# Kernel optimization log

Hardware: AMD Instinct MI355X
Metric: run time of the kernel (lower is better)

## Reference

```python
import jax, jax.numpy as jnp
import numpy as np

N, E, D = 50000, 400000, 64
L, NA, NS = 5, 4, 3            # layers, num aggregators, num scalers
ATOM_C, ATOM_V = 9, 64         # OGB-style atom feature columns / vocab
BOND_C, BOND_V = 3, 8
EPS = 1e-5
AVG_LOG = float(np.log(9.0))   # avg_d['log'] = ln(avg_degree + 1), avg_degree = 8


def setup_inputs() -> dict:
    key = jax.random.key(0)
    ks = jax.random.split(key, 8)
    x = jax.random.randint(ks[0], (N, ATOM_C), 0, ATOM_V)
    edge_index = jax.random.randint(ks[1], (2, E), 0, N)
    edge_attr = jax.random.randint(ks[2], (E, BOND_C), 0, BOND_V)
    init = lambda k, shape, fan: (jax.random.normal(k, shape, jnp.float32) / np.sqrt(fan))
    atom_emb = init(ks[3], (ATOM_C, ATOM_V, D), D)
    bond_emb = init(ks[4], (BOND_C, BOND_V, D), D)
    pre_W = init(ks[5], (L, 3 * D, D), 3 * D)                 # pretrans: Linear(3D -> D)
    pre_b = jnp.zeros((L, D), jnp.float32)
    post_W = init(ks[6], (L, (NA * NS + 1) * D, D), (NA * NS + 1) * D)  # posttrans: Linear(13D -> D)
    post_b = jnp.zeros((L, D), jnp.float32)
    return dict(x=x, edge_index=edge_index, edge_attr=edge_attr,
                atom_emb=atom_emb, bond_emb=bond_emb,
                pre_W=pre_W, pre_b=pre_b, post_W=post_W, post_b=post_b)


def reference(x, edge_index, edge_attr, atom_emb, bond_emb, pre_W, pre_b, post_W, post_b):
    src, dst = edge_index[0], edge_index[1]  # PyG: x_j = x[edge_index[0]], x_i = x[edge_index[1]]
    # Encoders: sum of per-column categorical embeddings (OGB Atom/BondEncoder)
    h0 = atom_emb[jnp.arange(ATOM_C)[None, :], x].sum(axis=1)        # [N, D]
    e = bond_emb[jnp.arange(BOND_C)[None, :], edge_attr].sum(axis=1)  # [E, D]
    # message input cat([x_i, x_j, edge_attr]) -- identical for every layer since
    # PNAGNN.forward never feeds layer output back in as x (faithful to source)
    z2 = jnp.concatenate([h0[dst], h0[src], e], axis=-1)              # [E, 3D]
    deg = jax.ops.segment_sum(jnp.ones((E,), jnp.float32), dst, num_segments=N)
    degc = jnp.maximum(deg, 1.0)[:, None]
    log_deg = jnp.log(jnp.maximum(deg, 1.0) + 1.0)[:, None]           # guard deg=0 for attenuation
    amp = log_deg / AVG_LOG
    att = AVG_LOG / log_deg
    has = (deg > 0)[:, None]
    h_in = h0
    for l in range(L):
        m = z2 @ pre_W[l] + pre_b[l]                                  # pretrans (1 layer, no act)
        s_sum = jax.ops.segment_sum(m, dst, num_segments=N)
        mean = s_sum / degc
        mx = jnp.where(has, jax.ops.segment_max(m, dst, num_segments=N), 0.0)
        mn = jnp.where(has, jax.ops.segment_min(m, dst, num_segments=N), 0.0)
        mean_sq = jax.ops.segment_sum(m * m, dst, num_segments=N) / degc
        var = jax.nn.relu(mean_sq - mean * mean)
        std = jnp.sqrt(var + EPS)
        agg = jnp.concatenate([mean, mx, mn, std], axis=-1)           # [N, 4D]
        scaled = jnp.concatenate([agg, agg * amp, agg * att], axis=-1)  # [N, 12D]
        hcat = jnp.concatenate([scaled, h0], axis=-1)                 # [N, 13D]
        out = hcat @ post_W[l] + post_b[l]                            # posttrans (1 layer, no act)
        h = out + h_in                                                # PNAGNN residual
        h_in = h
    return h
```

## Files before the change

kernel.cpp:

```cpp
#include <hip/hip_runtime.h>
#include <hip/hip_bf16.h>

#define NN 50000
#define NE 400000
#define AVG_LOG_F 2.1972245773362196f
#define EPSV 1e-5f

typedef __hip_bfloat16 bf16;
typedef __attribute__((ext_vector_type(8))) short short8v;
typedef __attribute__((ext_vector_type(4))) float f32x4;
typedef __attribute__((ext_vector_type(2))) _Float16 h2v;

__device__ __forceinline__ float b2f(bf16 v){ return __bfloat162float(v); }
__device__ __forceinline__ bf16  f2b(float v){ return __float2bfloat16(v); }
__device__ __forceinline__ short f2s(float v){
  bf16 b = __float2bfloat16(v);
  short s; __builtin_memcpy(&s, &b, 2); return s;
}
__device__ __forceinline__ short f2h(float v){
  _Float16 h = (_Float16)v;
  short s; __builtin_memcpy(&s, &h, 2); return s;
}

__global__ void k_h0(const int* __restrict__ x, const float* __restrict__ aemb,
                     bf16* __restrict__ h0b){
  int idx = blockIdx.x * 256 + threadIdx.x;
  if (idx >= NN * 64) return;
  int n = idx >> 6, d = idx & 63;
  float acc = 0.f;
  #pragma unroll
  for (int c = 0; c < 9; ++c){
    int a = x[n * 9 + c];
    acc += aemb[(c * 64 + a) * 64 + d];
  }
  h0b[idx] = f2b(acc);
}

__global__ void k_deg_code(const int* __restrict__ ei, const int* __restrict__ ea,
                           int* __restrict__ deg, int* __restrict__ code){
  int e = blockIdx.x * 256 + threadIdx.x;
  if (e >= NE) return;
  int dst = ei[NE + e];
  atomicAdd(&deg[dst], 1);
  code[e] = ea[e * 3] + 8 * ea[e * 3 + 1] + 64 * ea[e * 3 + 2];
}

__global__ void k_scan1(const int* __restrict__ deg, int* __restrict__ rowptr,
                        int* __restrict__ part){
  __shared__ int s[256];
  int t = threadIdx.x, i = blockIdx.x * 256 + t;
  int v = (i < NN) ? deg[i] : 0;
  s[t] = v; __syncthreads();
  for (int off = 1; off < 256; off <<= 1){
    int xv = (t >= off) ? s[t - off] : 0;
    __syncthreads();
    s[t] += xv;
    __syncthreads();
  }
  if (i < NN) rowptr[i] = s[t] - v;
  if (t == 255) part[blockIdx.x] = s[255];
}

__global__ void k_scan2(int* __restrict__ part, int nblk){
  __shared__ int s[256];
  int t = threadIdx.x;
  int v = (t < nblk) ? part[t] : 0;
  s[t] = v; __syncthreads();
  for (int off = 1; off < 256; off <<= 1){
    int xv = (t >= off) ? s[t - off] : 0;
    __syncthreads();
    s[t] += xv;
    __syncthreads();
  }
  if (t < nblk) part[t] = s[t] - v;
}

__global__ void k_scan3(int* __restrict__ rowptr, const int* __restrict__ part,
                        const int* __restrict__ deg, float* __restrict__ amp,
                        float* __restrict__ att){
  int i = blockIdx.x * 256 + threadIdx.x;
  if (i < NN){
    rowptr[i] += part[blockIdx.x];
    int d = deg[i];
    float ld = logf((float)max(d, 1) + 1.0f);
    amp[i] = ld / AVG_LOG_F;
    att[i] = AVG_LOG_F / ld;
  }
  if (i == 0) rowptr[NN] = NE;
}

__global__ void k_scatter(const int* __restrict__ ei, const int* __restrict__ code,
                          const int* __restrict__ rowptr, int* __restrict__ cursor,
                          int2* __restrict__ sedge){
  int e = blockIdx.x * 256 + threadIdx.x;
  if (e >= NE) return;
  int dst = ei[NE + e];
  int pos = rowptr[dst] + atomicAdd(&cursor[dst], 1);
  int2 v; v.x = ei[e] * 1280; v.y = code[e] * 640;
  sedge[pos] = v;
}

__global__ void k_ctab(const float* __restrict__ bemb, const float* __restrict__ preW,
                       _Float16* __restrict__ CTp){
  __shared__ float et[64];
  int cb = blockIdx.x, l = blockIdx.y, t = threadIdx.x;
  int a0 = cb & 7, a1 = (cb >> 3) & 7, a2 = (cb >> 6) & 7;
  et[t] = bemb[(0 * 8 + a0) * 64 + t] + bemb[(1 * 8 + a1) * 64 + t] + bemb[(2 * 8 + a2) * 64 + t];
  __syncthreads();
  float acc = 0.f;
  const float* W = preW + (l * 192 + 128) * 64;
  for (int k = 0; k < 64; ++k) acc += et[k] * W[k * 64 + t];
  char* base = (char*)CTp + (size_t)cb * 640;
  if (l < 4) *(short*)(base + t * 8 + l * 2) = f2h(acc);
  else       *(short*)(base + 512 + t * 2)   = f2h(acc);
}

__global__ void k_whsum(const float* __restrict__ postW, const float* __restrict__ postb,
                        float* __restrict__ whs, float* __restrict__ bs){
  int idx = blockIdx.x * 256 + threadIdx.x;
  if (idx < 4096){
    int k = idx >> 6, d = idx & 63;
    float a = 0.f;
    for (int l = 0; l < 5; ++l) a += postW[(size_t)(l * 832 + 768 + k) * 64 + d];
    whs[idx] = a;
  }
  if (idx < 64){
    float a = 0.f;
    for (int l = 0; l < 5; ++l) a += postb[l * 64 + idx];
    bs[idx] = a;
  }
}

__global__ void k_wtk(const float* __restrict__ postW, bf16* __restrict__ WtKf){
  int idx = blockIdx.x * 256 + threadIdx.x;
  if (idx >= 40 * 12 * 64 * 8) return;
  int s   = idx / 6144;
  int rem = idx % 6144;
  int gw  = rem / 512;
  int lane = (rem % 512) / 8;
  int j   = idx & 7;
  int g = gw >> 2, w4 = gw & 3;
  int kp = s * 32 + (lane >> 4) * 8 + j;
  int l = kp >> 8, kl = kp & 255;
  int c = w4 * 16 + (lane & 15);
  WtKf[idx] = f2b(postW[((size_t)l * 832 + g * 256 + kl) * 64 + c]);
}

__global__ void k_wtpre896(const float* __restrict__ preW, const float* __restrict__ preb,
                           const float* __restrict__ whs, const float* __restrict__ bs,
                           bf16* __restrict__ Wtp, float* __restrict__ bias896){
  int idx = blockIdx.x * 256 + threadIdx.x;
  if (idx < 896 * 64){
    int gc = idx >> 6, k = idx & 63;
    float v;
    if (gc < 320){
      int l = gc >> 6, c = gc & 63;
      v = preW[(size_t)(l * 192 + k) * 64 + c];
    } else if (gc < 832){
      int q = gc - 320, d = q >> 3, l = q & 7;
      v = (l < 5) ? preW[(size_t)(l * 192 + 64 + k) * 64 + d] : 0.f;
    } else {
      int c = gc - 832;
      v = whs[k * 64 + c] + ((k == c) ? 1.f : 0.f);
    }
    Wtp[idx] = f2b(v);
  }
  if (idx < 896){
    float b;
    if (idx < 320)      b = preb[(idx >> 6) * 64 + (idx & 63)];
    else if (idx < 832) b = 0.f;
    else                b = bs[idx - 832];
    bias896[idx] = b;
  }
}

__global__ __launch_bounds__(256) void k_ab_mfma(const bf16* __restrict__ h0b,
                                                 const bf16* __restrict__ Wtp,
                                                 const float* __restrict__ bias896,
                                                 char* __restrict__ ABU,
                                                 float* __restrict__ out){
  __shared__ bf16 As[128][72];
  __shared__ bf16 Bs[128][72];
  const int t = threadIdx.x;
  const int n0 = blockIdx.x * 128;
  const int gc0 = blockIdx.y * 128;
  const int lane = t & 63, wid = t >> 6;
  const int rw = wid * 32;
  const short* H  = (const short*)h0b;
  const short* Wp = (const short*)Wtp;

  #pragma unroll
  for (int i = 0; i < 4; ++i){
    int idx = t + i * 256;
    int r = idx >> 3, ko = (idx & 7) * 8;
    int n = n0 + r;
    short8v v = short8v{0,0,0,0,0,0,0,0};
    if (n < NN) v = *(const short8v*)(H + (size_t)n * 64 + ko);
    *(short8v*)&As[r][ko] = v;
  }
  #pragma unroll
  for (int i = 0; i < 4; ++i){
    int idx = t + i * 256;
    int cc = idx >> 3, ko = (idx & 7) * 8;
    *(short8v*)&Bs[cc][ko] = *(const short8v*)(Wp + (size_t)(gc0 + cc) * 64 + ko);
  }
  __syncthreads();

  f32x4 acc[2][8] = {};
  #pragma unroll
  for (int kk = 0; kk < 2; ++kk){
    short8v af0 = *(const short8v*)&As[rw + (lane & 15)][kk * 32 + (lane >> 4) * 8];
    short8v af1 = *(const short8v*)&As[rw + 16 + (lane & 15)][kk * 32 + (lane >> 4) * 8];
    #pragma unroll
    for (int j = 0; j < 8; ++j){
      short8v bfj = *(const short8v*)&Bs[j * 16 + (lane & 15)][kk * 32 + (lane >> 4) * 8];
      acc[0][j] = __builtin_amdgcn_mfma_f32_16x16x32_bf16(af0, bfj, acc[0][j], 0, 0, 0);
      acc[1][j] = __builtin_amdgcn_mfma_f32_16x16x32_bf16(af1, bfj, acc[1][j], 0, 0, 0);
    }
  }

  #pragma unroll
  for (int i = 0; i < 2; ++i){
    #pragma unroll
    for (int r = 0; r < 4; ++r){
      int n = n0 + rw + i * 16 + (lane >> 4) * 4 + r;
      if (n >= NN) continue;
      char* nb = ABU + (size_t)n * 1280;
      #pragma unroll
      for (int j = 0; j < 8; ++j){
        int gc = gc0 + j * 16 + (lane & 15);
        float v = acc[i][j][r] + bias896[gc];
        if (gc < 320){
          *(short*)(nb + gc * 2) = f2h(v);
        } else if (gc < 832){
          int q = gc - 320, dd = q >> 3, l = q & 7;
          if (l < 4)       *(short*)(nb + 640 + dd * 8 + l * 2) = f2h(v);
          else if (l == 4) *(short*)(nb + 1152 + dd * 2)        = f2h(v);
        } else {
          out[(size_t)n * 64 + (gc - 832)] = v;
        }
      }
    }
  }
}

__global__ __launch_bounds__(256) void k_gather(const char* __restrict__ ABU,
                                                const char* __restrict__ CTp,
                                                const int* __restrict__ rowptr,
                                                const int2* __restrict__ sedge,
                                                bf16* __restrict__ AGG){
  const int t = threadIdx.x, lane = t & 63, wid = t >> 6;
  const int n = blockIdx.x * 4 + wid;
  const char* AB8 = ABU + 640;
  const char* AB2 = ABU + 1152;
  const char* CT8 = CTp;
  const char* CT2 = CTp + 512;
  short* AGs = (short*)AGG;

  int r0 = rowptr[n], r1 = rowptr[n + 1];
  float s[5]  = {0.f, 0.f, 0.f, 0.f, 0.f};
  float sq[5] = {0.f, 0.f, 0.f, 0.f, 0.f};
  const _Float16 FLO = (_Float16)(-65504.f);
  const _Float16 FHI = (_Float16)( 65504.f);
  h2v mx01 = h2v{FLO, FLO}, mx23 = h2v{FLO, FLO};
  h2v mn01 = h2v{FHI, FHI}, mn23 = h2v{FHI, FHI};
  float mx4 = -65504.f, mn4 = 65504.f;

  union U8 { uint2 u; h2v h[2]; };
  const int l8 = lane * 8, l2 = lane * 2;

  for (int j = r0; j < r1; j += 4){
    int rem = r1 - j;
    int2 e0 = sedge[j];
    int2 e1 = (rem > 1) ? sedge[j + 1] : e0;
    int2 e2 = (rem > 2) ? sedge[j + 2] : e0;
    int2 e3 = (rem > 3) ? sedge[j + 3] : e0;
    U8 a0, a1, a2, a3, c0, c1, c2, c3;
    unsigned short b0, b1, b2, b3, d0, d1, d2, d3;
    a0.u = *(const uint2*)(AB8 + e0.x + l8);  b0 = *(const unsigned short*)(AB2 + e0.x + l2);
    c0.u = *(const uint2*)(CT8 + e0.y + l8);  d0 = *(const unsigned short*)(CT2 + e0.y + l2);
    a1.u = *(const uint2*)(AB8 + e1.x + l8);  b1 = *(const unsigned short*)(AB2 + e1.x + l2);
    c1.u = *(const uint2*)(CT8 + e1.y + l8);  d1 = *(const unsigned short*)(CT2 + e1.y + l2);
    a2.u = *(const uint2*)(AB8 + e2.x + l8);  b2 = *(const unsigned short*)(AB2 + e2.x + l2);
    c2.u = *(const uint2*)(CT8 + e2.y + l8);  d2 = *(const unsigned short*)(CT2 + e2.y + l2);
    a3.u = *(const uint2*)(AB8 + e3.x + l8);  b3 = *(const unsigned short*)(AB2 + e3.x + l2);
    c3.u = *(const uint2*)(CT8 + e3.y + l8);  d3 = *(const unsigned short*)(CT2 + e3.y + l2);

    #define EDGE_ACC(A, C, BL, DL) {                                \
      h2v t01 = A.h[0] + C.h[0];                                    \
      h2v t23 = A.h[1] + C.h[1];                                    \
      _Float16 hb, hd;                                              \
      __builtin_memcpy(&hb, &BL, 2);                                \
      __builtin_memcpy(&hd, &DL, 2);                                \
      float f4 = (float)(hb + hd);                                  \
      mx01 = __builtin_elementwise_max(mx01, t01);                  \
      mx23 = __builtin_elementwise_max(mx23, t23);                  \
      mn01 = __builtin_elementwise_min(mn01, t01);                  \
      mn23 = __builtin_elementwise_min(mn23, t23);                  \
      mx4 = fmaxf(mx4, f4); mn4 = fminf(mn4, f4);                   \
      float f0 = (float)t01[0], f1 = (float)t01[1];                 \
      float f2 = (float)t23[0], f3 = (float)t23[1];                 \
      s[0] += f0; sq[0] = fmaf(f0, f0, sq[0]);                      \
      s[1] += f1; sq[1] = fmaf(f1, f1, sq[1]);                      \
      s[2] += f2; sq[2] = fmaf(f2, f2, sq[2]);                      \
      s[3] += f3; sq[3] = fmaf(f3, f3, sq[3]);                      \
      s[4] += f4; sq[4] = fmaf(f4, f4, sq[4]);                      \
    }
    EDGE_ACC(a0, c0, b0, d0);
    if (rem > 1) EDGE_ACC(a1, c1, b1, d1);
    if (rem > 2) EDGE_ACC(a2, c2, b2, d2);
    if (rem > 3) EDGE_ACC(a3, c3, b3, d3);
    #undef EDGE_ACC
  }

  float mx[5] = {(float)mx01[0], (float)mx01[1], (float)mx23[0], (float)mx23[1], mx4};
  float mn[5] = {(float)mn01[0], (float)mn01[1], (float)mn23[0], (float)mn23[1], mn4};

  int d = r1 - r0;
  float degc = (float)((d > 0) ? d : 1);
  size_t base = (size_t)n * 1280;
  const char* nb = ABU + (size_t)n * 1280;
  #pragma unroll
  for (int l = 0; l < 5; ++l){
    _Float16 Kh; __builtin_memcpy(&Kh, nb + l * 128 + lane * 2, 2);
    float K = (float)Kh;
    float mean = ((float)d * K + s[l]) / degc;
    float MX = (d > 0) ? (K + mx[l]) : 0.f;
    float MN = (d > 0) ? (K + mn[l]) : 0.f;
    float mu = s[l] / degc;
    float var = fmaxf(sq[l] / degc - mu * mu, 0.f);
    float sd = sqrtf(var + EPSV);
    AGs[base + l * 256 + lane]       = f2s(mean);
    AGs[base + l * 256 + 64 + lane]  = f2s(MX);
    AGs[base + l * 256 + 128 + lane] = f2s(MN);
    AGs[base + l * 256 + 192 + lane] = f2s(sd);
  }
}

__global__ __launch_bounds__(256) void k_post5(const bf16* __restrict__ AGG,
                                               const bf16* __restrict__ WtKf,
                                               const float* __restrict__ amp,
                                               const float* __restrict__ att,
                                               float* __restrict__ out){
  const int t = threadIdx.x, lane = t & 63, w4 = t >> 6;
  const int rg0 = blockIdx.x * 2;
  const char* pa0 = (const char*)AGG +
      ((size_t)(rg0 * 16) + (lane & 15)) * 2560 + (lane >> 4) * 16;
  const char* pa1 = pa0 + 16 * 2560;
  const char* pb  = (const char*)WtKf + w4 * 1024 + lane * 16;

  f32x4 acc[2][3] = {};
  short8v A0a, A1a, B0a, B1a, B2a, A0b, A1b, B0b, B1b, B2b;
  A0a = *(const short8v*)pa0;
  A1a = *(const short8v*)pa1;
  B0a = *(const short8v*)pb;
  B1a = *(const short8v*)(pb + 4096);
  B2a = *(const short8v*)(pb + 8192);

  #define MFMA6(A0, A1, B0, B1, B2)                                          \
    acc[0][0] = __builtin_amdgcn_mfma_f32_16x16x32_bf16(A0, B0, acc[0][0], 0, 0, 0); \
    acc[0][1] = __builtin_amdgcn_mfma_f32_16x16x32_bf16(A0, B1, acc[0][1], 0, 0, 0); \
    acc[0][2] = __builtin_amdgcn_mfma_f32_16x16x32_bf16(A0, B2, acc[0][2], 0, 0, 0); \
    acc[1][0] = __builtin_amdgcn_mfma_f32_16x16x32_bf16(A1, B0, acc[1][0], 0, 0, 0); \
    acc[1][1] = __builtin_amdgcn_mfma_f32_16x16x32_bf16(A1, B1, acc[1][1], 0, 0, 0); \
    acc[1][2] = __builtin_amdgcn_mfma_f32_16x16x32_bf16(A1, B2, acc[1][2], 0, 0, 0);

  for (int k = 0; k < 19; ++k){
    A0b = *(const short8v*)(pa0 + 64);
    A1b = *(const short8v*)(pa1 + 64);
    B0b = *(const short8v*)(pb + 12288);
    B1b = *(const short8v*)(pb + 12288 + 4096);
    B2b = *(const short8v*)(pb + 12288 + 8192);
    MFMA6(A0a, A1a, B0a, B1a, B2a);
    pa0 += 128; pa1 += 128; pb += 24576;
    A0a = *(const short8v*)pa0;
    A1a = *(const short8v*)pa1;
    B0a = *(const short8v*)pb;
    B1a = *(const short8v*)(pb + 4096);
    B2a = *(const short8v*)(pb + 8192);
    MFMA6(A0b, A1b, B0b, B1b, B2b);
  }
  A0b = *(const short8v*)(pa0 + 64);
  A1b = *(const short8v*)(pa1 + 64);
  B0b = *(const short8v*)(pb + 12288);
  B1b = *(const short8v*)(pb + 12288 + 4096);
  B2b = *(const short8v*)(pb + 12288 + 8192);
  MFMA6(A0a, A1a, B0a, B1a, B2a);
  MFMA6(A0b, A1b, B0b, B1b, B2b);
  #undef MFMA6

  #pragma unroll
  for (int i = 0; i < 2; ++i){
    #pragma unroll
    for (int r = 0; r < 4; ++r){
      int n = (rg0 + i) * 16 + (lane >> 4) * 4 + r;
      if (n >= NN) continue;
      float am = amp[n], at = att[n];
      int c = w4 * 16 + (lane & 15);
      out[(size_t)n * 64 + c] += acc[i][0][r] + am * acc[i][1][r] + at * acc[i][2][r];
    }
  }
}

extern "C" void kernel_launch(void* const* d_in, const int* in_sizes, int n_in,
                              void* d_out, int out_size, void* d_ws, size_t ws_size,
                              hipStream_t stream){
  const int*   x     = (const int*)d_in[0];
  const int*   ei    = (const int*)d_in[1];
  const int*   ea    = (const int*)d_in[2];
  const float* aemb  = (const float*)d_in[3];
  const float* bemb  = (const float*)d_in[4];
  const float* preW  = (const float*)d_in[5];
  const float* preb  = (const float*)d_in[6];
  const float* postW = (const float*)d_in[7];
  const float* postb = (const float*)d_in[8];
  float* out = (float*)d_out;

  char* p = (char*)d_ws;
  auto alloc = [&](size_t bytes) -> char* {
    char* r = p;
    p += (bytes + 255) & ~(size_t)255;
    return r;
  };
  bf16*      h0b     = (bf16*)     alloc((size_t)NN * 64 * 2);
  char*      ABU     = (char*)     alloc((size_t)NN * 1280);
  bf16*      AGG     = (bf16*)     alloc((size_t)(NN + 16) * 1280 * 2);
  int*       deg     = (int*)      alloc((size_t)NN * 4);
  int*       rowptr  = (int*)      alloc((size_t)(NN + 1) * 4);
  int*       cursor  = (int*)      alloc((size_t)NN * 4);
  float*     amp     = (float*)    alloc((size_t)NN * 4);
  float*     att     = (float*)    alloc((size_t)NN * 4);
  int*       code    = (int*)      alloc((size_t)NE * 4);
  int2*      sedge   = (int2*)     alloc((size_t)NE * 8);
  _Float16*  CTp     = (_Float16*) alloc((size_t)512 * 640);
  float*     whs     = (float*)    alloc((size_t)64 * 64 * 4);
  float*     bs      = (float*)    alloc((size_t)64 * 4);
  int*       part    = (int*)      alloc((size_t)256 * 4);
  bf16*      WtKf    = (bf16*)     alloc((size_t)40 * 12 * 64 * 8 * 2);
  bf16*      Wtp     = (bf16*)     alloc((size_t)896 * 64 * 2);
  float*     bias896 = (float*)    alloc((size_t)896 * 4);
  if ((size_t)(p - (char*)d_ws) > ws_size) return;

  hipMemsetAsync(deg, 0, (size_t)NN * 4, stream);
  hipMemsetAsync(cursor, 0, (size_t)NN * 4, stream);

  k_h0<<<dim3((NN * 64 + 255) / 256), 256, 0, stream>>>(x, aemb, h0b);
  k_deg_code<<<dim3((NE + 255) / 256), 256, 0, stream>>>(ei, ea, deg, code);
  int nblk = (NN + 255) / 256;
  k_scan1<<<dim3(nblk), 256, 0, stream>>>(deg, rowptr, part);
  k_scan2<<<dim3(1), 256, 0, stream>>>(part, nblk);
  k_scan3<<<dim3(nblk), 256, 0, stream>>>(rowptr, part, deg, amp, att);
  k_scatter<<<dim3((NE + 255) / 256), 256, 0, stream>>>(ei, code, rowptr, cursor, sedge);
  k_ctab<<<dim3(512, 5), 64, 0, stream>>>(bemb, preW, CTp);
  k_whsum<<<dim3(16), 256, 0, stream>>>(postW, postb, whs, bs);
  k_wtk<<<dim3((40 * 12 * 64 * 8 + 255) / 256), 256, 0, stream>>>(postW, WtKf);
  k_wtpre896<<<dim3((896 * 64 + 255) / 256), 256, 0, stream>>>(preW, preb, whs, bs,
                                                               Wtp, bias896);
  k_ab_mfma<<<dim3((NN + 127) / 128, 7), 256, 0, stream>>>(h0b, Wtp, bias896, ABU, out);
  k_gather<<<dim3(NN / 4), 256, 0, stream>>>(ABU, (const char*)CTp, rowptr, sedge, AGG);
  k_post5<<<dim3((3125 + 1) / 2), 256, 0, stream>>>(AGG, WtKf, amp, att, out);
}
```

Baseline: 312.9 us.

## Store aggregates in MFMA fragment order and widen post GEMM tile to 64 rows

The gather kernel now handles 16 nodes per 1024-thread block, stages each node's aggregate row in shared memory, and writes it out pre-swizzled into the MFMA A-fragment layout, so the post GEMM reads fully contiguous 1 KB chunks instead of strided rows. The post GEMM covers four 16-row groups per block instead of two, so each loaded weight fragment is reused across more rows, with double-buffered register loads. The aim is to cut uncoalesced A loads and redundant weight traffic. In exchange it adds a shared-memory staging step with a block barrier, larger blocks in the gather, more accumulator registers, and a padded workspace buffer.

```diff
diff --git a/kernel.cpp b/kernel.cpp
--- a/kernel.cpp
+++ b/kernel.cpp
@@ -244,18 +244,18 @@
   }
 }
 
-__global__ __launch_bounds__(256) void k_gather(const char* __restrict__ ABU,
-                                                const char* __restrict__ CTp,
-                                                const int* __restrict__ rowptr,
-                                                const int2* __restrict__ sedge,
-                                                bf16* __restrict__ AGG){
+__global__ __launch_bounds__(1024, 8) void k_gather(const char* __restrict__ ABU,
+                                                    const char* __restrict__ CTp,
+                                                    const int* __restrict__ rowptr,
+                                                    const int2* __restrict__ sedge,
+                                                    bf16* __restrict__ AGGf){
+  __shared__ __align__(16) short ag[16][1288];
   const int t = threadIdx.x, lane = t & 63, wid = t >> 6;
-  const int n = blockIdx.x * 4 + wid;
+  const int n = blockIdx.x * 16 + wid;
   const char* AB8 = ABU + 640;
   const char* AB2 = ABU + 1152;
   const char* CT8 = CTp;
   const char* CT2 = CTp + 512;
-  short* AGs = (short*)AGG;
 
   int r0 = rowptr[n], r1 = rowptr[n + 1];
   float s[5]  = {0.f, 0.f, 0.f, 0.f, 0.f};
@@ -318,7 +318,6 @@
 
   int d = r1 - r0;
   float degc = (float)((d > 0) ? d : 1);
-  size_t base = (size_t)n * 1280;
   const char* nb = ABU + (size_t)n * 1280;
   #pragma unroll
   for (int l = 0; l < 5; ++l){
@@ -330,74 +329,79 @@
     float mu = s[l] / degc;
     float var = fmaxf(sq[l] / degc - mu * mu, 0.f);
     float sd = sqrtf(var + EPSV);
-    AGs[base + l * 256 + lane]       = f2s(mean);
-    AGs[base + l * 256 + 64 + lane]  = f2s(MX);
-    AGs[base + l * 256 + 128 + lane] = f2s(MN);
-    AGs[base + l * 256 + 192 + lane] = f2s(sd);
-  }
-}
-
-__global__ __launch_bounds__(256) void k_post5(const bf16* __restrict__ AGG,
-                                               const bf16* __restrict__ WtKf,
-                                               const float* __restrict__ amp,
-                                               const float* __restrict__ att,
-                                               float* __restrict__ out){
+    ag[wid][l * 256 + lane]       = f2s(mean);
+    ag[wid][l * 256 + 64 + lane]  = f2s(MX);
+    ag[wid][l * 256 + 128 + lane] = f2s(MN);
+    ag[wid][l * 256 + 192 + lane] = f2s(sd);
+  }
+  __syncthreads();
+
+  char* dst = (char*)AGGf + (size_t)blockIdx.x * 40960;
+  for (int c = t; c < 2560; c += 1024){
+    int ln = c & 63;
+    int row = ln & 15;
+    int k = (c >> 6) * 32 + (ln >> 4) * 8;
+    short8v v = *(const short8v*)&ag[row][k];
+    *(short8v*)(dst + (size_t)c * 16) = v;
+  }
+}
+
+__global__ __launch_bounds__(256, 2) void k_post5(const bf16* __restrict__ AGGf,
+                                                  const bf16* __restrict__ WtKf,
+                                                  const float* __restrict__ amp,
+                                                  const float* __restrict__ att,
+                                                  float* __restrict__ out){
   const int t = threadIdx.x, lane = t & 63, w4 = t >> 6;
-  const int rg0 = blockIdx.x * 2;
-  const char* pa0 = (const char*)AGG +
-      ((size_t)(rg0 * 16) + (lane & 15)) * 2560 + (lane >> 4) * 16;
-  const char* pa1 = pa0 + 16 * 2560;
-  const char* pb  = (const char*)WtKf + w4 * 1024 + lane * 16;
-
-  f32x4 acc[2][3] = {};
-  short8v A0a, A1a, B0a, B1a, B2a, A0b, A1b, B0b, B1b, B2b;
-  A0a = *(const short8v*)pa0;
-  A1a = *(const short8v*)pa1;
-  B0a = *(const short8v*)pb;
-  B1a = *(const short8v*)(pb + 4096);
-  B2a = *(const short8v*)(pb + 8192);
-
-  #define MFMA6(A0, A1, B0, B1, B2)                                          \
-    acc[0][0] = __builtin_amdgcn_mfma_f32_16x16x32_bf16(A0, B0, acc[0][0], 0, 0, 0); \
-    acc[0][1] = __builtin_amdgcn_mfma_f32_16x16x32_bf16(A0, B1, acc[0][1], 0, 0, 0); \
-    acc[0][2] = __builtin_amdgcn_mfma_f32_16x16x32_bf16(A0, B2, acc[0][2], 0, 0, 0); \
-    acc[1][0] = __builtin_amdgcn_mfma_f32_16x16x32_bf16(A1, B0, acc[1][0], 0, 0, 0); \
-    acc[1][1] = __builtin_amdgcn_mfma_f32_16x16x32_bf16(A1, B1, acc[1][1], 0, 0, 0); \
-    acc[1][2] = __builtin_amdgcn_mfma_f32_16x16x32_bf16(A1, B2, acc[1][2], 0, 0, 0);
-
+  const long g0 = (long)blockIdx.x * 4;
+  const char* pa = (const char*)AGGf + (size_t)g0 * 40960 + lane * 16;
+  const char* pb = (const char*)WtKf + w4 * 1024 + lane * 16;
+
+  f32x4 acc[4][3] = {};
+  short8v Ax[4], Bx[3], Ay[4], By[3];
+
+  #define LOADX(sidx) { \
+    _Pragma("unroll") for (int gi = 0; gi < 4; ++gi) \
+      Ax[gi] = *(const short8v*)(pa + (size_t)gi * 40960 + (size_t)(sidx) * 1024); \
+    _Pragma("unroll") for (int g = 0; g < 3; ++g) \
+      Bx[g] = *(const short8v*)(pb + (size_t)(sidx) * 12288 + g * 4096); }
+  #define LOADY(sidx) { \
+    _Pragma("unroll") for (int gi = 0; gi < 4; ++gi) \
+      Ay[gi] = *(const short8v*)(pa + (size_t)gi * 40960 + (size_t)(sidx) * 1024); \
+    _Pragma("unroll") for (int g = 0; g < 3; ++g) \
+      By[g] = *(const short8v*)(pb + (size_t)(sidx) * 12288 + g * 4096); }
+  #define MFMAX { \
+    _Pragma("unroll") for (int gi = 0; gi < 4; ++gi){ \
+      _Pragma("unroll") for (int g = 0; g < 3; ++g) \
+        acc[gi][g] = __builtin_amdgcn_mfma_f32_16x16x32_bf16(Ax[gi], Bx[g], acc[gi][g], 0, 0, 0); } }
+  #define MFMAY { \
+    _Pragma("unroll") for (int gi = 0; gi < 4; ++gi){ \
+      _Pragma("unroll") for (int g = 0; g < 3; ++g) \
+        acc[gi][g] = __builtin_amdgcn_mfma_f32_16x16x32_bf16(Ay[gi], By[g], acc[gi][g], 0, 0, 0); } }
+
+  LOADX(0);
+  LOADY(1);
   for (int k = 0; k < 19; ++k){
-    A0b = *(const short8v*)(pa0 + 64);
-    A1b = *(const short8v*)(pa1 + 64);
-    B0b = *(const short8v*)(pb + 12288);
-    B1b = *(const short8v*)(pb + 12288 + 4096);
-    B2b = *(const short8v*)(pb + 12288 + 8192);
-    MFMA6(A0a, A1a, B0a, B1a, B2a);
-    pa0 += 128; pa1 += 128; pb += 24576;
-    A0a = *(const short8v*)pa0;
-    A1a = *(const short8v*)pa1;
-    B0a = *(const short8v*)pb;
-    B1a = *(const short8v*)(pb + 4096);
-    B2a = *(const short8v*)(pb + 8192);
-    MFMA6(A0b, A1b, B0b, B1b, B2b);
-  }
-  A0b = *(const short8v*)(pa0 + 64);
-  A1b = *(const short8v*)(pa1 + 64);
-  B0b = *(const short8v*)(pb + 12288);
-  B1b = *(const short8v*)(pb + 12288 + 4096);
-  B2b = *(const short8v*)(pb + 12288 + 8192);
-  MFMA6(A0a, A1a, B0a, B1a, B2a);
-  MFMA6(A0b, A1b, B0b, B1b, B2b);
-  #undef MFMA6
-
-  #pragma unroll
-  for (int i = 0; i < 2; ++i){
+    MFMAX;
+    LOADX(2 * k + 2);
+    MFMAY;
+    LOADY(2 * k + 3);
+  }
+  MFMAX;
+  MFMAY;
+  #undef LOADX
+  #undef LOADY
+  #undef MFMAX
+  #undef MFMAY
+
+  #pragma unroll
+  for (int gi = 0; gi < 4; ++gi){
     #pragma unroll
     for (int r = 0; r < 4; ++r){
-      int n = (rg0 + i) * 16 + (lane >> 4) * 4 + r;
+      long n = (g0 + gi) * 16 + (lane >> 4) * 4 + r;
       if (n >= NN) continue;
       float am = amp[n], at = att[n];
       int c = w4 * 16 + (lane & 15);
-      out[(size_t)n * 64 + c] += acc[i][0][r] + am * acc[i][1][r] + at * acc[i][2][r];
+      out[(size_t)n * 64 + c] += acc[gi][0][r] + am * acc[gi][1][r] + at * acc[gi][2][r];
     }
   }
 }
@@ -424,7 +428,7 @@
   };
   bf16*      h0b     = (bf16*)     alloc((size_t)NN * 64 * 2);
   char*      ABU     = (char*)     alloc((size_t)NN * 1280);
-  bf16*      AGG     = (bf16*)     alloc((size_t)(NN + 16) * 1280 * 2);
+  bf16*      AGGf    = (bf16*)     alloc((size_t)3128 * 40960);
   int*       deg     = (int*)      alloc((size_t)NN * 4);
   int*       rowptr  = (int*)      alloc((size_t)(NN + 1) * 4);
   int*       cursor  = (int*)      alloc((size_t)NN * 4);
@@ -457,6 +461,6 @@
   k_wtpre896<<<dim3((896 * 64 + 255) / 256), 256, 0, stream>>>(preW, preb, whs, bs,
                                                                Wtp, bias896);
   k_ab_mfma<<<dim3((NN + 127) / 128, 7), 256, 0, stream>>>(h0b, Wtp, bias896, ABU, out);
-  k_gather<<<dim3(NN / 4), 256, 0, stream>>>(ABU, (const char*)CTp, rowptr, sedge, AGG);
-  k_post5<<<dim3((3125 + 1) / 2), 256, 0, stream>>>(AGG, WtKf, amp, att, out);
-}
+  k_gather<<<dim3(NN / 16), 1024, 0, stream>>>(ABU, (const char*)CTp, rowptr, sedge, AGGf);
+  k_post5<<<dim3(782), 256, 0, stream>>>(AGGf, WtKf, amp, att, out);
+}
```

After: 277.4 us. 11.3% less time.
